# Kernel tuning notes

Measured on AMD Instinct MI355X. Metric: run time of the kernel, lower is better.

Reference implementation:

```python
import jax, jax.numpy as jnp
import numpy as np

N = 40960          # total nodes in batch of session graphs
S = 4096           # number of sessions (segments)
E = 81920          # directed edges
D = 64             # embedding_dim
H = 100            # hidden_dim
F_IN = 5 * D + 1   # 321, price + 5 concatenated embeddings
V_ITEMS = 50000
NUM_ITER = 1


def setup_inputs() -> dict:
    key = jax.random.key(0)
    ks = jax.random.split(key, 30)
    rn = lambda k, shape, s=0.05: (jax.random.normal(k, shape, jnp.float32) * s)
    ri = lambda k, shape, hi: jax.random.randint(k, shape, 0, hi, jnp.int64)
    return {
        "price": rn(ks[0], (N, 1), 1.0),
        "category": ri(ks[1], (N,), 256),
        "sub_category": ri(ks[2], (N,), 1024),
        "element": ri(ks[3], (N,), 2048),
        "brand": ri(ks[4], (N,), 4096),
        "product_id": ri(ks[5], (N,), V_ITEMS),
        "edge_index": ri(ks[6], (2, E), N),
        "batch": jnp.repeat(jnp.arange(S, dtype=jnp.int64), N // S),  # sorted segment ids, 10 nodes/session
        "emb_cat": rn(ks[7], (256, D)),
        "emb_sub": rn(ks[8], (1024, D)),
        "emb_elem": rn(ks[9], (2048, D)),
        "emb_brand": rn(ks[10], (4096, D)),
        "emb_item": rn(ks[11], (V_ITEMS, D)),
        "W_msg": rn(ks[12], (F_IN, H)),
        "b_msg": rn(ks[13], (H,)),
        "W_ih": rn(ks[14], (H, 3 * H)),
        "W_hh": rn(ks[15], (H, 3 * H)),
        "b_ih": rn(ks[16], (3 * H,)),
        "b_hh": rn(ks[17], (3 * H,)),
        "W_last": rn(ks[18], (F_IN, H)),
        "b_last": rn(ks[19], (H,)),
        "W_g1": rn(ks[20], (H, H)),
        "b_g1": rn(ks[21], (H,)),
        "W_g2": rn(ks[22], (H, 1)),
        "b_g2": rn(ks[23], (1,)),
        "W_fc": rn(ks[24], (H, V_ITEMS)),
        "b_fc": rn(ks[25], (V_ITEMS,)),
    }


def _gru_cell(x, h, W_ih, W_hh, b_ih, b_hh):
    # torch.nn.GRUCell math, gates ordered [r, z, n]
    gi = x @ W_ih + b_ih                     # [N, 3H]
    gh = h @ W_hh + b_hh                     # [N, 3H]
    i_r, i_z, i_n = jnp.split(gi, 3, axis=1)
    h_r, h_z, h_n = jnp.split(gh, 3, axis=1)
    r = jax.nn.sigmoid(i_r + h_r)
    z = jax.nn.sigmoid(i_z + h_z)
    n = jnp.tanh(i_n + r * h_n)
    return (1.0 - z) * n + z * h


def reference(price, category, sub_category, element, brand, product_id,
              edge_index, batch,
              emb_cat, emb_sub, emb_elem, emb_brand, emb_item,
              W_msg, b_msg, W_ih, W_hh, b_ih, b_hh,
              W_last, b_last, W_g1, b_g1, W_g2, b_g2, W_fc, b_fc):
    # ----- NodeEmbedding: 5 gathers + price concat -> [N, 321] -----
    x = jnp.concatenate([
        price,
        emb_cat[category], emb_sub[sub_category], emb_elem[element],
        emb_brand[brand], emb_item[product_id],
    ], axis=1)

    # ----- GRUGraphLayer: message_linear, then mean-aggregate + GRUCell -----
    h = x @ W_msg + b_msg                                     # [N, H]
    src, dst = edge_index[0], edge_index[1]
    deg = jax.ops.segment_sum(jnp.ones((E,), jnp.float32), dst, num_segments=N)
    inv_deg = jnp.where(deg > 0, 1.0 / jnp.maximum(deg, 1.0), 0.0)[:, None]
    for _ in range(NUM_ITER):
        msg = jax.ops.segment_sum(h[src], dst, num_segments=N) * inv_deg  # mean aggr
        h = _gru_cell(msg, h, W_ih, W_hh, b_ih, b_hh)

    # ----- last-visited node per session (scatter_max on arange -> last index) -----
    last_idx = jax.ops.segment_max(jnp.arange(N, dtype=jnp.int64), batch, num_segments=S)
    last = x[last_idx] @ W_last + b_last                       # [S, H]
    h = h + last[batch]                                        # broadcast back to nodes

    # ----- AttentionalAggregation: gate MLP + segment softmax + weighted sum -----
    # (dropout is inference no-op)
    gate = (jax.nn.relu(h @ W_g1 + b_g1) @ W_g2 + b_g2)[:, 0]  # [N]
    gmax = jax.ops.segment_max(gate, batch, num_segments=S)
    w = jnp.exp(gate - gmax[batch])
    wsum = jax.ops.segment_sum(w, batch, num_segments=S)
    alpha = w / wsum[batch]                                    # [N]
    pooled = jax.ops.segment_sum(alpha[:, None] * h, batch, num_segments=S)  # [S, H]

    # ----- final scoring over item catalog -----
    return pooled @ W_fc + b_fc                                # [S, V_ITEMS]
```

## Files before the change

kernel.cpp:

```cpp
#include <hip/hip_runtime.h>
#include <hip/hip_bf16.h>

#define N_NODES 40960
#define N_SESS  4096
#define N_EDGES 81920
#define DIM     64
#define HID     100
#define VITEMS  50000

typedef short s16x8 __attribute__((ext_vector_type(8)));
typedef float f32x4 __attribute__((ext_vector_type(4)));

__device__ __forceinline__ unsigned short f2bf(float f) {
    unsigned u = __float_as_uint(f);
    return (unsigned short)((u + 0x7FFFu + ((u >> 16) & 1u)) >> 16);
}
__device__ __forceinline__ float bf2f(unsigned short s) {
    return __uint_as_float(((unsigned)s) << 16);
}

__global__ __launch_bounds__(256)
void gemm_f32(const float* __restrict__ A, int lda,
              const float* __restrict__ B, int ldb,
              const float* __restrict__ bias,
              float* __restrict__ C, int ldc,
              int M, int N, int K, int relu)
{
    __shared__ float As[32][68];
    __shared__ float Bs[32][68];
    const int tid = threadIdx.x;
    const int tm = tid & 15;
    const int tn = tid >> 4;
    const int m0 = blockIdx.y * 64;
    const int n0 = blockIdx.x * 64;
    float acc[4][4] = {};

    for (int k0 = 0; k0 < K; k0 += 32) {
        #pragma unroll
        for (int i = 0; i < 2; ++i) {
            int f4  = tid + i * 256;
            int row = f4 >> 3;
            int kc  = (f4 & 7) << 2;
            float4 v = make_float4(0.f, 0.f, 0.f, 0.f);
            int gm = m0 + row, gk = k0 + kc;
            if (gm < M && gk < K)
                v = *reinterpret_cast<const float4*>(&A[(size_t)gm * lda + gk]);
            As[kc + 0][row] = v.x;
            As[kc + 1][row] = v.y;
            As[kc + 2][row] = v.z;
            As[kc + 3][row] = v.w;
        }
        #pragma unroll
        for (int i = 0; i < 2; ++i) {
            int f4  = tid + i * 256;
            int row = f4 >> 4;
            int nc  = (f4 & 15) << 2;
            float4 v = make_float4(0.f, 0.f, 0.f, 0.f);
            int gk = k0 + row, gn = n0 + nc;
            if (gk < K && gn < N)
                v = *reinterpret_cast<const float4*>(&B[(size_t)gk * ldb + gn]);
            *reinterpret_cast<float4*>(&Bs[row][nc]) = v;
        }
        __syncthreads();
        #pragma unroll
        for (int kk = 0; kk < 32; ++kk) {
            float4 a4 = *reinterpret_cast<const float4*>(&As[kk][tm << 2]);
            float4 b4 = *reinterpret_cast<const float4*>(&Bs[kk][tn << 2]);
            float av[4] = {a4.x, a4.y, a4.z, a4.w};
            float bv[4] = {b4.x, b4.y, b4.z, b4.w};
            #pragma unroll
            for (int i = 0; i < 4; ++i)
                #pragma unroll
                for (int j = 0; j < 4; ++j)
                    acc[i][j] += av[i] * bv[j];
        }
        __syncthreads();
    }

    const int gn0 = n0 + (tn << 2);
    if (gn0 >= N) return;
    float4 bi = make_float4(0.f, 0.f, 0.f, 0.f);
    if (bias) bi = *reinterpret_cast<const float4*>(&bias[gn0]);
    #pragma unroll
    for (int i = 0; i < 4; ++i) {
        int gm = m0 + (tm << 2) + i;
        if (gm >= M) continue;
        float4 o = make_float4(acc[i][0] + bi.x, acc[i][1] + bi.y,
                               acc[i][2] + bi.z, acc[i][3] + bi.w);
        if (relu) {
            o.x = fmaxf(o.x, 0.f); o.y = fmaxf(o.y, 0.f);
            o.z = fmaxf(o.z, 0.f); o.w = fmaxf(o.w, 0.f);
        }
        *reinterpret_cast<float4*>(&C[(size_t)gm * ldc + gn0]) = o;
    }
}

__global__ __launch_bounds__(256)
void b_split(const float* __restrict__ Wfc, unsigned short* __restrict__ Bh,
             unsigned short* __restrict__ Bl)
{
    __shared__ unsigned short Hs[64][136];
    __shared__ unsigned short Ls[64][136];
    const int n0 = blockIdx.x * 64;
    const int nn = threadIdx.x & 63, kk = threadIdx.x >> 6;
    for (int k = kk; k < 128; k += 4) {
        float v = 0.f;
        int n = n0 + nn;
        if (k < HID && n < VITEMS) v = Wfc[(size_t)k * VITEMS + n];
        unsigned short h = f2bf(v);
        Hs[nn][k] = h;
        Ls[nn][k] = f2bf(v - bf2f(h));
    }
    __syncthreads();
    const int row = threadIdx.x >> 2, part = threadIdx.x & 3;
    size_t base = (size_t)(n0 + row) * 128 + part * 32;
    #pragma unroll
    for (int c = 0; c < 4; ++c) {
        *reinterpret_cast<s16x8*>(&Bh[base + c * 8]) =
            *reinterpret_cast<const s16x8*>(&Hs[row][part * 32 + c * 8]);
        *reinterpret_cast<s16x8*>(&Bl[base + c * 8]) =
            *reinterpret_cast<const s16x8*>(&Ls[row][part * 32 + c * 8]);
    }
}

__global__ void a_split(const float* __restrict__ pooled, unsigned short* __restrict__ Ah,
                        unsigned short* __restrict__ Al)
{
    int idx = blockIdx.x * 256 + threadIdx.x;
    if (idx >= N_SESS * 128) return;
    int m = idx >> 7, k = idx & 127;
    float v = (k < HID) ? pooled[m * HID + k] : 0.f;
    unsigned short h = f2bf(v);
    Ah[idx] = h;
    Al[idx] = f2bf(v - bf2f(h));
}

__global__ __launch_bounds__(256)
void score_gemm(const unsigned short* __restrict__ Ah, const unsigned short* __restrict__ Al,
                const unsigned short* __restrict__ Bh, const unsigned short* __restrict__ Bl,
                const float* __restrict__ bias, float* __restrict__ out)
{
    const int chunk = blockIdx.x & 7;
    const int m0    = (blockIdx.x >> 3) * 64;
    const int w     = threadIdx.x >> 6;
    const int l     = threadIdx.x & 63;
    const int lm    = l & 15;
    const int lk    = l >> 4;

    s16x8 ah[4][4], al[4][4];
    #pragma unroll
    for (int mf = 0; mf < 4; ++mf)
        #pragma unroll
        for (int ks = 0; ks < 4; ++ks) {
            size_t off = (size_t)(m0 + mf * 16 + lm) * 128 + ks * 32 + lk * 8;
            ah[mf][ks] = *reinterpret_cast<const s16x8*>(Ah + off);
            al[mf][ks] = *reinterpret_cast<const s16x8*>(Al + off);
        }

    const int t0 = chunk * 98;
    const int t1 = (t0 + 98 < 782) ? t0 + 98 : 782;
    for (int nt = t0; nt < t1; ++nt) {
        const int n0 = nt * 64 + w * 16;
        f32x4 acc[4];
        #pragma unroll
        for (int mf = 0; mf < 4; ++mf) acc[mf] = (f32x4){0.f, 0.f, 0.f, 0.f};

        #pragma unroll
        for (int ks = 0; ks < 4; ++ks) {
            size_t boff = (size_t)(n0 + lm) * 128 + ks * 32 + lk * 8;
            s16x8 bh = *reinterpret_cast<const s16x8*>(Bh + boff);
            s16x8 bl = *reinterpret_cast<const s16x8*>(Bl + boff);
            #pragma unroll
            for (int mf = 0; mf < 4; ++mf) {
                acc[mf] = __builtin_amdgcn_mfma_f32_16x16x32_bf16(ah[mf][ks], bh, acc[mf], 0, 0, 0);
                acc[mf] = __builtin_amdgcn_mfma_f32_16x16x32_bf16(al[mf][ks], bh, acc[mf], 0, 0, 0);
                acc[mf] = __builtin_amdgcn_mfma_f32_16x16x32_bf16(ah[mf][ks], bl, acc[mf], 0, 0, 0);
            }
        }

        const int n = n0 + lm;
        if (n < VITEMS) {
            const float bv = bias[n];
            #pragma unroll
            for (int mf = 0; mf < 4; ++mf) {
                const int mbase = m0 + mf * 16 + lk * 4;
                #pragma unroll
                for (int r = 0; r < 4; ++r)
                    out[(size_t)(mbase + r) * VITEMS + n] = acc[mf][r] + bv;
            }
        }
    }
}

__global__ void h0_gather(const float* __restrict__ price,
                          const int* __restrict__ cat, const int* __restrict__ sub,
                          const int* __restrict__ elem, const int* __restrict__ brand,
                          const int* __restrict__ pid,
                          const float* __restrict__ Wmsg, const float* __restrict__ b_msg,
                          const float* __restrict__ Pm, float* __restrict__ h0)
{
    int idx = blockIdx.x * 256 + threadIdx.x;
    if (idx >= N_NODES * HID) return;
    int n = idx / HID, j = idx - n * HID;
    float v = b_msg[j] + price[n] * Wmsg[j];
    v += Pm[(size_t)(        cat[n]) * HID + j];
    v += Pm[(size_t)( 256 +  sub[n]) * HID + j];
    v += Pm[(size_t)(1280 + elem[n]) * HID + j];
    v += Pm[(size_t)(3328 + brand[n]) * HID + j];
    v += Pm[(size_t)(7424 +  pid[n]) * HID + j];
    h0[idx] = v;
}

__global__ void deg_count(const int* __restrict__ dst, float* __restrict__ deg)
{
    int e = blockIdx.x * 256 + threadIdx.x;
    if (e < N_EDGES) atomicAdd(&deg[dst[e]], 1.0f);
}

__global__ void inv_deg_k(float* __restrict__ deg)
{
    int n = blockIdx.x * 256 + threadIdx.x;
    if (n < N_NODES) {
        float d = deg[n];
        deg[n] = d > 0.f ? 1.0f / d : 0.0f;
    }
}

__global__ void msg_scatter(const int* __restrict__ src, const int* __restrict__ dst,
                            const float* __restrict__ h0, float* __restrict__ msg)
{
    int idx = blockIdx.x * 256 + threadIdx.x;
    if (idx >= N_EDGES * HID) return;
    int e = idx / HID, j = idx - e * HID;
    atomicAdd(&msg[(size_t)dst[e] * HID + j], h0[(size_t)src[e] * HID + j]);
}

__global__ void msg_scale(const float* __restrict__ inv_deg, float* __restrict__ msg)
{
    int idx = blockIdx.x * 256 + threadIdx.x;
    if (idx >= N_NODES * HID) return;
    int n = idx / HID;
    msg[idx] *= inv_deg[n];
}

__global__ void gru_gates(const float* __restrict__ gi, const float* __restrict__ gh,
                          float* __restrict__ h)
{
    int idx = blockIdx.x * 256 + threadIdx.x;
    if (idx >= 10240 * HID) return;
    int nl = idx / HID, j = idx - nl * HID;
    float ir  = gi[nl * 300 + j],        hr = gh[nl * 300 + j];
    float iz  = gi[nl * 300 + 100 + j],  hz = gh[nl * 300 + 100 + j];
    float in_ = gi[nl * 300 + 200 + j],  hn = gh[nl * 300 + 200 + j];
    float r  = 1.f / (1.f + expf(-(ir + hr)));
    float z  = 1.f / (1.f + expf(-(iz + hz)));
    float nn = tanhf(in_ + r * hn);
    float hv = h[idx];
    h[idx] = (1.f - z) * nn + z * hv;
}

__global__ void last_idx_k(const int* __restrict__ batch, int* __restrict__ last_idx)
{
    int n = blockIdx.x * 256 + threadIdx.x;
    if (n < N_NODES) atomicMax(&last_idx[batch[n]], n);
}

__global__ __launch_bounds__(256)
void last_proj(const int* __restrict__ last_idx, const float* __restrict__ price,
               const int* __restrict__ cat, const int* __restrict__ sub,
               const int* __restrict__ elem, const int* __restrict__ brand,
               const int* __restrict__ pid,
               const float* __restrict__ Ecat, const float* __restrict__ Esub,
               const float* __restrict__ Eelem, const float* __restrict__ Ebrand,
               const float* __restrict__ Eitem,
               const float* __restrict__ W_last, const float* __restrict__ b_last,
               float* __restrict__ last)
{
    int s = blockIdx.x * 4 + (threadIdx.x >> 6);
    int l = threadIdx.x & 63;
    int n = last_idx[s];
    int ci = cat[n] * DIM, si = sub[n] * DIM, ei = elem[n] * DIM;
    int bi = brand[n] * DIM, pi = pid[n] * DIM;
    float acc0 = 0.f, acc1 = 0.f;
    for (int k = 0; k < 321; ++k) {
        float xk;
        if (k == 0)       xk = price[n];
        else if (k < 65)  xk = Ecat[ci + k - 1];
        else if (k < 129) xk = Esub[si + k - 65];
        else if (k < 193) xk = Eelem[ei + k - 129];
        else if (k < 257) xk = Ebrand[bi + k - 193];
        else              xk = Eitem[pi + k - 257];
        acc0 += xk * W_last[k * HID + l];
        if (l < HID - 64) acc1 += xk * W_last[k * HID + 64 + l];
    }
    last[s * HID + l] = acc0 + b_last[l];
    if (l < HID - 64) last[s * HID + 64 + l] = acc1 + b_last[64 + l];
}

__global__ void add_last(const int* __restrict__ batch, const float* __restrict__ last,
                         float* __restrict__ h)
{
    int idx = blockIdx.x * 256 + threadIdx.x;
    if (idx >= N_NODES * HID) return;
    int n = idx / HID, j = idx - n * HID;
    h[idx] += last[(size_t)batch[n] * HID + j];
}

__global__ __launch_bounds__(256)
void gate_reduce(const float* __restrict__ g1, const float* __restrict__ W_g2,
                 const float* __restrict__ b_g2, const int* __restrict__ batch,
                 float* __restrict__ gate, unsigned* __restrict__ gmax)
{
    int n = blockIdx.x * 4 + (threadIdx.x >> 6);
    int l = threadIdx.x & 63;
    float s = g1[(size_t)n * HID + l] * W_g2[l];
    if (l < HID - 64) s += g1[(size_t)n * HID + 64 + l] * W_g2[64 + l];
    #pragma unroll
    for (int off = 32; off > 0; off >>= 1) s += __shfl_xor(s, off, 64);
    if (l == 0) {
        float gt = s + b_g2[0];
        gate[n] = gt;
        unsigned u = __float_as_uint(gt);
        u = (u & 0x80000000u) ? ~u : (u | 0x80000000u);
        atomicMax(&gmax[batch[n]], u);
    }
}

__global__ void softmax_w(const int* __restrict__ batch, const unsigned* __restrict__ gmax,
                          float* __restrict__ gate, float* __restrict__ wsum)
{
    int n = blockIdx.x * 256 + threadIdx.x;
    if (n >= N_NODES) return;
    unsigned u = gmax[batch[n]];
    float gm = (u & 0x80000000u) ? __uint_as_float(u ^ 0x80000000u) : __uint_as_float(~u);
    float w = expf(gate[n] - gm);
    gate[n] = w;
    atomicAdd(&wsum[batch[n]], w);
}

__global__ void pooled_k(const int* __restrict__ batch, const float* __restrict__ gate,
                         const float* __restrict__ wsum, const float* __restrict__ h,
                         float* __restrict__ pooled)
{
    int idx = blockIdx.x * 256 + threadIdx.x;
    if (idx >= N_NODES * HID) return;
    int n = idx / HID, j = idx - n * HID;
    int b = batch[n];
    float alpha = gate[n] / wsum[b];
    atomicAdd(&pooled[(size_t)b * HID + j], alpha * h[idx]);
}

extern "C" void kernel_launch(void* const* d_in, const int* in_sizes, int n_in,
                              void* d_out, int out_size, void* d_ws, size_t ws_size,
                              hipStream_t stream)
{
    const float* price    = (const float*)d_in[0];
    const int*   cat      = (const int*)d_in[1];
    const int*   sub      = (const int*)d_in[2];
    const int*   elem     = (const int*)d_in[3];
    const int*   brand    = (const int*)d_in[4];
    const int*   pid      = (const int*)d_in[5];
    const int*   eidx     = (const int*)d_in[6];
    const int*   batch    = (const int*)d_in[7];
    const float* emb_cat  = (const float*)d_in[8];
    const float* emb_sub  = (const float*)d_in[9];
    const float* emb_elem = (const float*)d_in[10];
    const float* emb_brand= (const float*)d_in[11];
    const float* emb_item = (const float*)d_in[12];
    const float* W_msg    = (const float*)d_in[13];
    const float* b_msg    = (const float*)d_in[14];
    const float* W_ih     = (const float*)d_in[15];
    const float* W_hh     = (const float*)d_in[16];
    const float* b_ih     = (const float*)d_in[17];
    const float* b_hh     = (const float*)d_in[18];
    const float* W_last   = (const float*)d_in[19];
    const float* b_last   = (const float*)d_in[20];
    const float* W_g1     = (const float*)d_in[21];
    const float* b_g1     = (const float*)d_in[22];
    const float* W_g2     = (const float*)d_in[23];
    const float* b_g2     = (const float*)d_in[24];
    const float* W_fc     = (const float*)d_in[25];
    const float* b_fc     = (const float*)d_in[26];
    float* out = (float*)d_out;

    const int* src = eidx;
    const int* dst = eidx + N_EDGES;

    float* w = (float*)d_ws;
    float*    msg    = w + 0;
    float*    deg    = w + 4096000;
    float*    wsum   = w + 4136960;
    float*    pooled = w + 4141056;
    int*      lastix = (int*)(w + 4550656);
    unsigned* gmax   = (unsigned*)(w + 4554752);
    float*    Pm     = w + 4558848;
    float*    h0     = w + 10301248;
    float*    gi     = w + 14397248;
    float*    gh     = w + 17469248;
    float*    last   = w + 20541248;
    float*    gate   = w + 20950848;

    unsigned short* Bth = (unsigned short*)msg;
    unsigned short* Btl = (unsigned short*)gi;
    unsigned short* Ahp = (unsigned short*)Pm;
    unsigned short* Alp = (unsigned short*)(Pm + 262144);

    hipMemsetAsync(w, 0, (size_t)4558848 * sizeof(float), stream);

    dim3 blk(256);
    auto gemm = [&](const float* A, int lda, const float* B, int ldb,
                    const float* bias, float* C, int ldc, int M, int N, int K, int relu) {
        dim3 g((N + 63) / 64, (M + 63) / 64);
        hipLaunchKernelGGL(gemm_f32, g, blk, 0, stream, A, lda, B, ldb, bias, C, ldc, M, N, K, relu);
    };

    gemm(emb_cat,   DIM, W_msg +   1 * HID, HID, nullptr, Pm +      0, HID,   256, HID, DIM, 0);
    gemm(emb_sub,   DIM, W_msg +  65 * HID, HID, nullptr, Pm +  25600, HID,  1024, HID, DIM, 0);
    gemm(emb_elem,  DIM, W_msg + 129 * HID, HID, nullptr, Pm + 128000, HID,  2048, HID, DIM, 0);
    gemm(emb_brand, DIM, W_msg + 193 * HID, HID, nullptr, Pm + 332800, HID,  4096, HID, DIM, 0);
    gemm(emb_item,  DIM, W_msg + 257 * HID, HID, nullptr, Pm + 742400, HID, VITEMS, HID, DIM, 0);

    h0_gather<<<16000, blk, 0, stream>>>(price, cat, sub, elem, brand, pid, W_msg, b_msg, Pm, h0);

    deg_count<<<320, blk, 0, stream>>>(dst, deg);
    inv_deg_k<<<160, blk, 0, stream>>>(deg);
    msg_scatter<<<32000, blk, 0, stream>>>(src, dst, h0, msg);
    msg_scale<<<16000, blk, 0, stream>>>(deg, msg);

    for (int c = 0; c < 4; ++c) {
        size_t nb = (size_t)c * 10240;
        gemm(msg + nb * HID, HID, W_ih, 300, b_ih, gi, 300, 10240, 300, HID, 0);
        gemm(h0  + nb * HID, HID, W_hh, 300, b_hh, gh, 300, 10240, 300, HID, 0);
        gru_gates<<<4000, blk, 0, stream>>>(gi, gh, h0 + nb * HID);
    }

    last_idx_k<<<160, blk, 0, stream>>>(batch, lastix);
    last_proj<<<1024, blk, 0, stream>>>(lastix, price, cat, sub, elem, brand, pid,
                                        emb_cat, emb_sub, emb_elem, emb_brand, emb_item,
                                        W_last, b_last, last);
    add_last<<<16000, blk, 0, stream>>>(batch, last, h0);

    gemm(h0, HID, W_g1, HID, b_g1, msg , HID, N_NODES, HID, HID, 1);
    gate_reduce<<<10240, blk, 0, stream>>>(msg, W_g2, b_g2, batch, gate, gmax);

    b_split<<<782, blk, 0, stream>>>(W_fc, Bth, Btl);

    softmax_w<<<160, blk, 0, stream>>>(batch, gmax, gate, wsum);
    pooled_k<<<16000, blk, 0, stream>>>(batch, gate, wsum, h0, pooled);

    a_split<<<2048, blk, 0, stream>>>(pooled, Ahp, Alp);
    score_gemm<<<512, blk, 0, stream>>>(Ahp, Alp, Bth, Btl, b_fc, out);
}
```

Before: 1.778 ms.

## Fuse GRU GEMMs and gates into one split-bf16 MFMA kernel; prefetch B in score GEMM

The per-chunk fp32 GEMMs for W_ih and W_hh and the separate gate kernel are replaced by a single kernel. It splits msg and h0 into bf16 hi/lo pairs and computes both gate projections with three-term MFMA, keeping results in shared memory before applying the gate math. The score GEMM also gets register double-buffering of B fragments so the next tile's loads overlap the current MFMAs. This adds split/pad passes and more register pressure, and it relies on the bf16x3 split to stay close to fp32 accuracy.

```diff
diff --git a/kernel.cpp b/kernel.cpp
--- a/kernel.cpp
+++ b/kernel.cpp
@@ -123,16 +123,94 @@
     }
 }
 
-__global__ void a_split(const float* __restrict__ pooled, unsigned short* __restrict__ Ah,
-                        unsigned short* __restrict__ Al)
-{
-    int idx = blockIdx.x * 256 + threadIdx.x;
-    if (idx >= N_SESS * 128) return;
+__global__ void split_pad128(const float* __restrict__ in, int M,
+                             unsigned short* __restrict__ H, unsigned short* __restrict__ L)
+{
+    int idx = blockIdx.x * 256 + threadIdx.x;
+    if (idx >= M * 128) return;
     int m = idx >> 7, k = idx & 127;
-    float v = (k < HID) ? pooled[m * HID + k] : 0.f;
+    float v = (k < HID) ? in[(size_t)m * HID + k] : 0.f;
     unsigned short h = f2bf(v);
-    Ah[idx] = h;
-    Al[idx] = f2bf(v - bf2f(h));
+    H[idx] = h;
+    L[idx] = f2bf(v - bf2f(h));
+}
+
+__global__ void wtab_split(const float* __restrict__ Wih, const float* __restrict__ Whh,
+                           unsigned short* __restrict__ T)
+{
+    int idx = blockIdx.x * 256 + threadIdx.x;
+    if (idx >= 2 * 304 * 128) return;
+    int mat = idx / 38912;
+    int rem = idx - mat * 38912;
+    int n = rem >> 7, k = rem & 127;
+    const float* W = mat ? Whh : Wih;
+    float v = (k < HID && n < 300) ? W[(size_t)k * 300 + n] : 0.f;
+    unsigned short h = f2bf(v);
+    T[(size_t)(mat * 2) * 38912 + rem]     = h;
+    T[(size_t)(mat * 2 + 1) * 38912 + rem] = f2bf(v - bf2f(h));
+}
+
+__global__ __launch_bounds__(256)
+void gru_fused(const unsigned short* __restrict__ MsgH, const unsigned short* __restrict__ MsgL,
+               const unsigned short* __restrict__ H0H,  const unsigned short* __restrict__ H0L,
+               const unsigned short* __restrict__ Wtab,
+               const float* __restrict__ b_ih, const float* __restrict__ b_hh,
+               float* __restrict__ h)
+{
+    __shared__ float Gs[2][32][306];
+    const int nb = blockIdx.x * 32;
+    const int w  = threadIdx.x >> 6;
+    const int l  = threadIdx.x & 63;
+    const int lm = l & 15, lk = l >> 4;
+    const int mat = w >> 1;
+    const int mf  = w & 1;
+
+    const unsigned short* Ah = mat ? H0H : MsgH;
+    const unsigned short* Al = mat ? H0L : MsgL;
+    const unsigned short* Bh = Wtab + (size_t)(mat * 2) * 38912;
+    const unsigned short* Bl = Bh + 38912;
+
+    s16x8 ah[4], al[4];
+    #pragma unroll
+    for (int ks = 0; ks < 4; ++ks) {
+        size_t off = (size_t)(nb + mf * 16 + lm) * 128 + ks * 32 + lk * 8;
+        ah[ks] = *reinterpret_cast<const s16x8*>(Ah + off);
+        al[ks] = *reinterpret_cast<const s16x8*>(Al + off);
+    }
+
+    for (int nt = 0; nt < 19; ++nt) {
+        f32x4 acc = (f32x4){0.f, 0.f, 0.f, 0.f};
+        #pragma unroll
+        for (int ks = 0; ks < 4; ++ks) {
+            size_t boff = (size_t)(nt * 16 + lm) * 128 + ks * 32 + lk * 8;
+            s16x8 bh = *reinterpret_cast<const s16x8*>(Bh + boff);
+            s16x8 bl = *reinterpret_cast<const s16x8*>(Bl + boff);
+            acc = __builtin_amdgcn_mfma_f32_16x16x32_bf16(ah[ks], bh, acc, 0, 0, 0);
+            acc = __builtin_amdgcn_mfma_f32_16x16x32_bf16(al[ks], bh, acc, 0, 0, 0);
+            acc = __builtin_amdgcn_mfma_f32_16x16x32_bf16(ah[ks], bl, acc, 0, 0, 0);
+        }
+        #pragma unroll
+        for (int r = 0; r < 4; ++r)
+            Gs[mat][mf * 16 + lk * 4 + r][nt * 16 + lm] = acc[r];
+    }
+    __syncthreads();
+
+    for (int idx = threadIdx.x; idx < 3200; idx += 256) {
+        int node = idx / 100;
+        int j = idx - node * 100;
+        float ir  = Gs[0][node][j]       + b_ih[j];
+        float hr  = Gs[1][node][j]       + b_hh[j];
+        float iz  = Gs[0][node][100 + j] + b_ih[100 + j];
+        float hz  = Gs[1][node][100 + j] + b_hh[100 + j];
+        float in_ = Gs[0][node][200 + j] + b_ih[200 + j];
+        float hn  = Gs[1][node][200 + j] + b_hh[200 + j];
+        float r  = 1.f / (1.f + expf(-(ir + hr)));
+        float z  = 1.f / (1.f + expf(-(iz + hz)));
+        float nn = tanhf(in_ + r * hn);
+        size_t g = (size_t)(nb + node) * HID + j;
+        float hv = h[g];
+        h[g] = (1.f - z) * nn + z * hv;
+    }
 }
 
 __global__ __launch_bounds__(256)
@@ -159,26 +237,40 @@
 
     const int t0 = chunk * 98;
     const int t1 = (t0 + 98 < 782) ? t0 + 98 : 782;
+
+    s16x8 bh[4], bl[4];
+    #pragma unroll
+    for (int ks = 0; ks < 4; ++ks) {
+        size_t boff = (size_t)(t0 * 64 + w * 16 + lm) * 128 + ks * 32 + lk * 8;
+        bh[ks] = *reinterpret_cast<const s16x8*>(Bh + boff);
+        bl[ks] = *reinterpret_cast<const s16x8*>(Bl + boff);
+    }
+
     for (int nt = t0; nt < t1; ++nt) {
-        const int n0 = nt * 64 + w * 16;
+        const int ntn = (nt + 1 < t1) ? nt + 1 : nt;
+        s16x8 nbh[4], nbl[4];
+        #pragma unroll
+        for (int ks = 0; ks < 4; ++ks) {
+            size_t boff = (size_t)(ntn * 64 + w * 16 + lm) * 128 + ks * 32 + lk * 8;
+            nbh[ks] = *reinterpret_cast<const s16x8*>(Bh + boff);
+            nbl[ks] = *reinterpret_cast<const s16x8*>(Bl + boff);
+        }
+
         f32x4 acc[4];
         #pragma unroll
         for (int mf = 0; mf < 4; ++mf) acc[mf] = (f32x4){0.f, 0.f, 0.f, 0.f};
 
         #pragma unroll
         for (int ks = 0; ks < 4; ++ks) {
-            size_t boff = (size_t)(n0 + lm) * 128 + ks * 32 + lk * 8;
-            s16x8 bh = *reinterpret_cast<const s16x8*>(Bh + boff);
-            s16x8 bl = *reinterpret_cast<const s16x8*>(Bl + boff);
             #pragma unroll
             for (int mf = 0; mf < 4; ++mf) {
-                acc[mf] = __builtin_amdgcn_mfma_f32_16x16x32_bf16(ah[mf][ks], bh, acc[mf], 0, 0, 0);
-                acc[mf] = __builtin_amdgcn_mfma_f32_16x16x32_bf16(al[mf][ks], bh, acc[mf], 0, 0, 0);
-                acc[mf] = __builtin_amdgcn_mfma_f32_16x16x32_bf16(ah[mf][ks], bl, acc[mf], 0, 0, 0);
+                acc[mf] = __builtin_amdgcn_mfma_f32_16x16x32_bf16(ah[mf][ks], bh[ks], acc[mf], 0, 0, 0);
+                acc[mf] = __builtin_amdgcn_mfma_f32_16x16x32_bf16(al[mf][ks], bh[ks], acc[mf], 0, 0, 0);
+                acc[mf] = __builtin_amdgcn_mfma_f32_16x16x32_bf16(ah[mf][ks], bl[ks], acc[mf], 0, 0, 0);
             }
         }
 
-        const int n = n0 + lm;
+        const int n = nt * 64 + w * 16 + lm;
         if (n < VITEMS) {
             const float bv = bias[n];
             #pragma unroll
@@ -189,6 +281,9 @@
                     out[(size_t)(mbase + r) * VITEMS + n] = acc[mf][r] + bv;
             }
         }
+
+        #pragma unroll
+        for (int ks = 0; ks < 4; ++ks) { bh[ks] = nbh[ks]; bl[ks] = nbl[ks]; }
     }
 }
 
@@ -241,22 +336,6 @@
     if (idx >= N_NODES * HID) return;
     int n = idx / HID;
     msg[idx] *= inv_deg[n];
-}
-
-__global__ void gru_gates(const float* __restrict__ gi, const float* __restrict__ gh,
-                          float* __restrict__ h)
-{
-    int idx = blockIdx.x * 256 + threadIdx.x;
-    if (idx >= 10240 * HID) return;
-    int nl = idx / HID, j = idx - nl * HID;
-    float ir  = gi[nl * 300 + j],        hr = gh[nl * 300 + j];
-    float iz  = gi[nl * 300 + 100 + j],  hz = gh[nl * 300 + 100 + j];
-    float in_ = gi[nl * 300 + 200 + j],  hn = gh[nl * 300 + 200 + j];
-    float r  = 1.f / (1.f + expf(-(ir + hr)));
-    float z  = 1.f / (1.f + expf(-(iz + hz)));
-    float nn = tanhf(in_ + r * hn);
-    float hv = h[idx];
-    h[idx] = (1.f - z) * nn + z * hv;
 }
 
 __global__ void last_idx_k(const int* __restrict__ batch, int* __restrict__ last_idx)
@@ -400,10 +479,15 @@
     float*    last   = w + 20541248;
     float*    gate   = w + 20950848;
 
-    unsigned short* Bth = (unsigned short*)msg;
-    unsigned short* Btl = (unsigned short*)gi;
-    unsigned short* Ahp = (unsigned short*)Pm;
-    unsigned short* Alp = (unsigned short*)(Pm + 262144);
+    unsigned short* MsgH = (unsigned short*)gi;
+    unsigned short* MsgL = (unsigned short*)gh;
+    unsigned short* Wtab = (unsigned short*)(gh + 2621440);
+    unsigned short* H0H  = (unsigned short*)Pm;
+    unsigned short* H0L  = (unsigned short*)(Pm + 2621440);
+    unsigned short* Bth  = (unsigned short*)msg;
+    unsigned short* Btl  = (unsigned short*)gi;
+    unsigned short* Ahp  = (unsigned short*)Pm;
+    unsigned short* Alp  = (unsigned short*)(Pm + 262144);
 
     hipMemsetAsync(w, 0, (size_t)4558848 * sizeof(float), stream);
 
@@ -427,12 +511,10 @@
     msg_scatter<<<32000, blk, 0, stream>>>(src, dst, h0, msg);
     msg_scale<<<16000, blk, 0, stream>>>(deg, msg);
 
-    for (int c = 0; c < 4; ++c) {
-        size_t nb = (size_t)c * 10240;
-        gemm(msg + nb * HID, HID, W_ih, 300, b_ih, gi, 300, 10240, 300, HID, 0);
-        gemm(h0  + nb * HID, HID, W_hh, 300, b_hh, gh, 300, 10240, 300, HID, 0);
-        gru_gates<<<4000, blk, 0, stream>>>(gi, gh, h0 + nb * HID);
-    }
+    split_pad128<<<20480, blk, 0, stream>>>(msg, N_NODES, MsgH, MsgL);
+    split_pad128<<<20480, blk, 0, stream>>>(h0,  N_NODES, H0H,  H0L);
+    wtab_split<<<304, blk, 0, stream>>>(W_ih, W_hh, Wtab);
+    gru_fused<<<1280, blk, 0, stream>>>(MsgH, MsgL, H0H, H0L, Wtab, b_ih, b_hh, h0);
 
     last_idx_k<<<160, blk, 0, stream>>>(batch, lastix);
     last_proj<<<1024, blk, 0, stream>>>(lastix, price, cat, sub, elem, brand, pid,
@@ -448,6 +530,6 @@
     softmax_w<<<160, blk, 0, stream>>>(batch, gmax, gate, wsum);
     pooled_k<<<16000, blk, 0, stream>>>(batch, gate, wsum, h0, pooled);
 
-    a_split<<<2048, blk, 0, stream>>>(pooled, Ahp, Alp);
+    split_pad128<<<2048, blk, 0, stream>>>(pooled, N_SESS, Ahp, Alp);
     score_gemm<<<512, blk, 0, stream>>>(Ahp, Alp, Bth, Btl, b_fc, out);
 }
```

After: 1.615 ms. 1.1x faster.
